# Kernel tuning notes

Hardware: AMD Instinct MI355X
Metric: run time of the kernel (lower is better)

Reference implementation:

```python
import jax, jax.numpy as jnp
import numpy as np

B, N, C, H = 4, 4096, 1024, 16
HD = C // H  # head_dim = 64
EPS = 1e-6


def setup_inputs() -> dict:
    key = jax.random.key(0)
    ks = jax.random.split(key, 5)
    x = jax.random.normal(ks[0], (B, N, C), dtype=jnp.float32)
    s_in = 1.0 / np.sqrt(C)
    W_qkv = jax.random.normal(ks[1], (C, 3 * C), dtype=jnp.float32) * s_in
    b_qkv = jnp.zeros((3 * C,), dtype=jnp.float32)
    W_out = jax.random.normal(ks[2], (C, C), dtype=jnp.float32) * s_in
    b_out = jnp.zeros((C,), dtype=jnp.float32)
    return {"x": x, "W_qkv": W_qkv, "b_qkv": b_qkv, "W_out": W_out, "b_out": b_out}


def reference(x, W_qkv, b_qkv, W_out, b_out):
    # qkv projection: (B, N, 3C)
    qkv = jnp.einsum('bnc,cf->bnf', x, W_qkv) + b_qkv
    # rearrange 'b n (h d) -> b h n d' with d = 3*head_dim, then chunk into q,k,v
    qkv = qkv.reshape(B, N, H, 3 * HD).transpose(0, 2, 1, 3)  # (B,H,N,3*HD)
    q, k, v = jnp.split(qkv, 3, axis=-1)  # each (B,H,N,HD)
    # silu feature map
    q = jax.nn.silu(q)
    k = jax.nn.silu(k)
    # linear attention: state = k^T @ v per head  -> (B,H,HD,HD)
    state = jnp.einsum('bhnd,bhne->bhde', k, v)
    k_sum = k.sum(axis=2)  # (B,H,HD)
    num = jnp.einsum('bhnd,bhde->bhne', q, state)  # (B,H,N,HD)
    den = jnp.einsum('bhnd,bhd->bhn', q, k_sum)[..., None]  # (B,H,N,1)
    out = num / (den + EPS)
    # 'b h n d -> b n (h d)'
    out = out.transpose(0, 2, 1, 3).reshape(B, N, C)
    return jnp.einsum('bnc,cf->bnf', out, W_out) + b_out
```

## Files before the change

kernel.cpp:

```cpp
#include <hip/hip_runtime.h>

typedef unsigned short u16;
typedef unsigned int u32;
typedef __attribute__((ext_vector_type(8))) short short8;
typedef __attribute__((ext_vector_type(8))) _Float16 half8;
typedef __attribute__((ext_vector_type(4))) float f32x4;

#define DEV __device__ __forceinline__

DEV void async_copy16(const void* g, void* l) {
  __builtin_amdgcn_global_load_lds((const __attribute__((address_space(1))) u32*)g,
                                   (__attribute__((address_space(3))) u32*)l, 16, 0, 0);
}
DEV float bf2f(u16 u) { return __uint_as_float(((u32)u) << 16); }
DEV u16 f2bf(float f) {
  u32 x = __float_as_uint(f);
  return (u16)((x + 0x7fffu + ((x >> 16) & 1u)) >> 16);
}
DEV u16 f2h_bits(float f) { _Float16 h = (_Float16)f; return __builtin_bit_cast(u16, h); }
DEV float h2f_bits(u16 b) { return (float)__builtin_bit_cast(_Float16, b); }
DEV float silu_f(float x) { return x / (1.0f + __expf(-x)); }

DEV void stage_tile(const u16* __restrict__ G, size_t grow_base, int k0, u16* L, int t) {
#pragma unroll
  for (int it = 0; it < 2; ++it) {
    int c = t + it * 256;
    int r = c >> 2, j = c & 3;
    int js = j ^ ((r >> 1) & 3);
    async_copy16(G + ((grow_base + (size_t)r) << 10) + k0 + js * 8,
                 (char*)L + (size_t)c * 16);
  }
}
DEV half8 frag(const u16* L, int rr, int lq) {
  int sw = lq ^ ((rr >> 1) & 3);
  return *(const half8*)((const char*)L + (size_t)rr * 64 + sw * 16);
}
DEV short8 frag_s(const u16* L, int rr, int lq) {
  int sw = lq ^ ((rr >> 1) & 3);
  return *(const short8*)((const char*)L + (size_t)rr * 64 + sw * 16);
}
DEV half8 frag64(const u16* L, int rr, int slot) {
  return *(const half8*)(L + (size_t)rr * 64 + ((slot ^ (rr & 7)) * 8));
}

__global__ __launch_bounds__(256) void transpose_k(const float* __restrict__ W,
                                                   u16* __restrict__ Wt,
                                                   int K, int N) {
  __shared__ float s[32][33];
  int t = threadIdx.x;
  int tx = t & 31, ty = t >> 5;
  int ntk = K >> 5;
  int bk = blockIdx.x % ntk, bn = blockIdx.x / ntk;
  int k0 = bk * 32, n0 = bn * 32;
#pragma unroll
  for (int i = 0; i < 4; ++i)
    s[ty + 8 * i][tx] = W[(size_t)(k0 + ty + 8 * i) * N + n0 + tx];
  __syncthreads();
#pragma unroll
  for (int i = 0; i < 4; ++i) {
    int r = ty + 8 * i;
    Wt[(size_t)(n0 + r) * K + k0 + tx] = f2bf(s[tx][r]);
  }
}

__global__ __launch_bounds__(256) void prep(const float* __restrict__ x,
                                            u16* __restrict__ X0, u16* __restrict__ X1,
                                            const float* __restrict__ Wq,
                                            u16* __restrict__ W0t, u16* __restrict__ W1t,
                                            const float* __restrict__ Wo,
                                            u16* __restrict__ WoT) {
  __shared__ float s[32][33];
  int bid = blockIdx.x, t = threadIdx.x;
  if (bid < 16384) {
    int i = (bid * 256 + t) * 4;
    float4 v = *(const float4*)&x[i];
    ushort4 h0, h1;
    h0.x = f2h_bits(v.x); h1.x = f2h_bits((v.x - h2f_bits(h0.x)) * 4096.0f);
    h0.y = f2h_bits(v.y); h1.y = f2h_bits((v.y - h2f_bits(h0.y)) * 4096.0f);
    h0.z = f2h_bits(v.z); h1.z = f2h_bits((v.z - h2f_bits(h0.z)) * 4096.0f);
    h0.w = f2h_bits(v.w); h1.w = f2h_bits((v.w - h2f_bits(h0.w)) * 4096.0f);
    *(ushort4*)&X0[i] = h0;
    *(ushort4*)&X1[i] = h1;
  } else if (bid < 16384 + 3072) {
    int b2 = bid - 16384;
    int tx = t & 31, ty = t >> 5;
    int bk = b2 & 31, bn = b2 >> 5;
    int k0 = bk * 32, n0 = bn * 32;
#pragma unroll
    for (int i = 0; i < 4; ++i)
      s[ty + 8 * i][tx] = Wq[(size_t)(k0 + ty + 8 * i) * 3072 + n0 + tx];
    __syncthreads();
#pragma unroll
    for (int i = 0; i < 4; ++i) {
      int r = ty + 8 * i;
      int col = n0 + r;
      int h = col / 192, rem = col - h * 192;
      int cty = rem >> 6, d = rem & 63;
      int pcol = cty * 1024 + h * 64 + d;
      float v = s[tx][r];
      u16 h0 = f2h_bits(v);
      u16 h1 = f2h_bits((v - h2f_bits(h0)) * 4096.0f);
      size_t o = (size_t)pcol * 1024 + k0 + tx;
      W0t[o] = h0;
      W1t[o] = h1;
    }
  } else {
    int b3 = bid - 19456;
    int tx = t & 31, ty = t >> 5;
    int bk = b3 & 31, bn = b3 >> 5;
    int k0 = bk * 32, n0 = bn * 32;
#pragma unroll
    for (int i = 0; i < 4; ++i)
      s[ty + 8 * i][tx] = Wo[(size_t)(k0 + ty + 8 * i) * 1024 + n0 + tx];
    __syncthreads();
#pragma unroll
    for (int i = 0; i < 4; ++i) {
      int r = ty + 8 * i;
      WoT[(size_t)(n0 + r) * 1024 + k0 + tx] = f2bf(s[tx][r]);
    }
  }
}

__global__ __launch_bounds__(256, 2) void gemm_qk_f16(
    const u16* __restrict__ X0, const u16* __restrict__ X1,
    const u16* __restrict__ W0, const u16* __restrict__ W1,
    const float* __restrict__ bq,
    float* __restrict__ Qf, float* __restrict__ Kf) {
  __shared__ u16 lA0[128 * 32];
  __shared__ u16 lA1[128 * 32];
  __shared__ u16 lB0[128 * 32];
  __shared__ u16 lB1[128 * 32];
  int t = threadIdx.x;
  int w = t >> 6, l = t & 63;
  int wr = w >> 1, wc = w & 1;
  int lr = l & 15, lq = l >> 4;
  int mb = blockIdx.y * 128, nb = blockIdx.x * 128;
  int cty = nb >> 10;
  f32x4 aM[4][4] = {};
  f32x4 aC[4][4] = {};

  for (int k0 = 0; k0 < 1024; k0 += 32) {
#pragma unroll
    for (int it = 0; it < 2; ++it) {
      int c = t + it * 256;
      int r = c >> 2, j = c & 3;
      int js = j ^ ((r >> 1) & 3);
      size_t goA = (((size_t)(mb + r)) << 10) + k0 + js * 8;
      size_t goB = (((size_t)(nb + r)) << 10) + k0 + js * 8;
      async_copy16(X0 + goA, (char*)lA0 + (size_t)c * 16);
      async_copy16(X1 + goA, (char*)lA1 + (size_t)c * 16);
      async_copy16(W0 + goB, (char*)lB0 + (size_t)c * 16);
      async_copy16(W1 + goB, (char*)lB1 + (size_t)c * 16);
    }
    __syncthreads();
    half8 b0[4], b1[4];
#pragma unroll
    for (int nn = 0; nn < 4; ++nn) {
      int rr = wc * 64 + nn * 16 + lr;
      b0[nn] = frag(lB0, rr, lq);
      b1[nn] = frag(lB1, rr, lq);
    }
#pragma unroll
    for (int m = 0; m < 4; ++m) {
      int rr = wr * 64 + m * 16 + lr;
      half8 a0 = frag(lA0, rr, lq);
      half8 a1 = frag(lA1, rr, lq);
#pragma unroll
      for (int nn = 0; nn < 4; ++nn) {
        aM[m][nn] = __builtin_amdgcn_mfma_f32_16x16x32_f16(a0, b0[nn], aM[m][nn], 0, 0, 0);
        aC[m][nn] = __builtin_amdgcn_mfma_f32_16x16x32_f16(a0, b1[nn], aC[m][nn], 0, 0, 0);
        aC[m][nn] = __builtin_amdgcn_mfma_f32_16x16x32_f16(a1, b0[nn], aC[m][nn], 0, 0, 0);
      }
    }
    __syncthreads();
  }

  const float cscale = 2.44140625e-4f;
  float* dst = (cty == 0) ? Qf : Kf;
#pragma unroll
  for (int nn = 0; nn < 4; ++nn) {
    int col = nb + wc * 64 + nn * 16 + lr;
    int h = (col & 1023) >> 6, d0 = col & 63;
    float bias = bq[h * 192 + cty * 64 + d0];
#pragma unroll
    for (int m = 0; m < 4; ++m)
#pragma unroll
      for (int j = 0; j < 4; ++j) {
        int row = mb + wr * 64 + m * 16 + lq * 4 + j;
        int b = row >> 12, n = row & 4095;
        size_t base = (((size_t)(b * 16 + h) * 4096 + n) << 6) + d0;
        float val = aM[m][nn][j] + aC[m][nn][j] * cscale + bias;
        dst[base] = silu_f(val);
      }
  }
}

__global__ __launch_bounds__(256) void gemm_v_f16(
    const u16* __restrict__ X0, const u16* __restrict__ W0,
    const float* __restrict__ bq, u16* __restrict__ Vb) {
  __shared__ u16 lA0[128 * 32];
  __shared__ u16 lB0[128 * 32];
  int t = threadIdx.x;
  int w = t >> 6, l = t & 63;
  int wr = w >> 1, wc = w & 1;
  int lr = l & 15, lq = l >> 4;
  int mb = blockIdx.y * 128, nb = 2048 + blockIdx.x * 128;
  f32x4 aM[4][4] = {};

  for (int k0 = 0; k0 < 1024; k0 += 32) {
    stage_tile(X0, mb, k0, lA0, t);
    stage_tile(W0, nb, k0, lB0, t);
    __syncthreads();
    half8 b0[4];
#pragma unroll
    for (int nn = 0; nn < 4; ++nn) b0[nn] = frag(lB0, wc * 64 + nn * 16 + lr, lq);
#pragma unroll
    for (int m = 0; m < 4; ++m) {
      half8 a0 = frag(lA0, wr * 64 + m * 16 + lr, lq);
#pragma unroll
      for (int nn = 0; nn < 4; ++nn)
        aM[m][nn] = __builtin_amdgcn_mfma_f32_16x16x32_f16(a0, b0[nn], aM[m][nn], 0, 0, 0);
    }
    __syncthreads();
  }
#pragma unroll
  for (int nn = 0; nn < 4; ++nn) {
    int col = nb + wc * 64 + nn * 16 + lr;
    int h = (col & 1023) >> 6, d0 = col & 63;
    float bias = bq[h * 192 + 128 + d0];
#pragma unroll
    for (int m = 0; m < 4; ++m)
#pragma unroll
      for (int j = 0; j < 4; ++j) {
        int row = mb + wr * 64 + m * 16 + lq * 4 + j;
        int b = row >> 12, n = row & 4095;
        size_t base = (((size_t)(b * 16 + h) * 4096 + n) << 6) + d0;
        Vb[base] = f2bf(aM[m][nn][j] + bias);
      }
  }
}

__global__ __launch_bounds__(256) void gemm_qkv(const float* __restrict__ X,
                                                const float* __restrict__ Wq,
                                                const float* __restrict__ bq,
                                                float* __restrict__ Qf,
                                                float* __restrict__ Kf,
                                                u16* __restrict__ Vb) {
  __shared__ float sA[16 * 132];
  __shared__ float sB[16 * 128];
  int t = threadIdx.x;
  int tm = t >> 4, tn = t & 15;
  int mb = blockIdx.y * 128, nb = blockIdx.x * 128;
  float acc[8][8] = {};

  for (int k0 = 0; k0 < 1024; k0 += 16) {
#pragma unroll
    for (int it = 0; it < 2; ++it) {
      int c = t + it * 256;
      int m = c >> 2, kc = (c & 3) * 4;
      float4 v = *(const float4*)&X[(size_t)(mb + m) * 1024 + k0 + kc];
      sA[(kc + 0) * 132 + m] = v.x;
      sA[(kc + 1) * 132 + m] = v.y;
      sA[(kc + 2) * 132 + m] = v.z;
      sA[(kc + 3) * 132 + m] = v.w;
      int kr = c >> 5, nc = (c & 31) * 4;
      async_copy16(&Wq[(size_t)(k0 + kr) * 3072 + nb + nc], (char*)sB + (size_t)c * 16);
    }
    __syncthreads();
#pragma unroll
    for (int k = 0; k < 16; ++k) {
      float4 a0 = *(const float4*)&sA[k * 132 + tm * 8];
      float4 a1 = *(const float4*)&sA[k * 132 + tm * 8 + 4];
      float4 b0 = *(const float4*)&sB[k * 128 + tn * 8];
      float4 b1 = *(const float4*)&sB[k * 128 + tn * 8 + 4];
      const float av[8] = {a0.x, a0.y, a0.z, a0.w, a1.x, a1.y, a1.z, a1.w};
      const float bv[8] = {b0.x, b0.y, b0.z, b0.w, b1.x, b1.y, b1.z, b1.w};
#pragma unroll
      for (int i = 0; i < 8; ++i)
#pragma unroll
        for (int j = 0; j < 8; ++j) acc[i][j] = fmaf(av[i], bv[j], acc[i][j]);
    }
    __syncthreads();
  }

  int c0 = nb + tn * 8;
  int h = c0 / 192, rem = c0 % 192;
  int ty = rem >> 6, d0 = rem & 63;
  float bb[8];
#pragma unroll
  for (int j = 0; j < 8; ++j) bb[j] = bq[c0 + j];
#pragma unroll
  for (int i = 0; i < 8; ++i) {
    int r = mb + tm * 8 + i;
    int b = r >> 12, n = r & 4095;
    size_t base = (((size_t)(b * 16 + h) * 4096 + n) << 6) + d0;
    if (ty == 2) {
      u16 pk[8];
#pragma unroll
      for (int j = 0; j < 8; ++j) pk[j] = f2bf(acc[i][j] + bb[j]);
      *(short8*)&Vb[base] = *(short8*)pk;
    } else {
      float* dst = (ty == 0) ? Qf : Kf;
#pragma unroll
      for (int j = 0; j < 8; ++j) dst[base + j] = silu_f(acc[i][j] + bb[j]);
    }
  }
}

__global__ __launch_bounds__(256) void state_partial(const float* __restrict__ Kf,
                                                     const u16* __restrict__ Vb,
                                                     float* __restrict__ stateP,
                                                     float* __restrict__ ksumP) {
  int bh = blockIdx.y, ch = blockIdx.x, t = threadIdx.x;
  __shared__ float sK[64 * 64];
  __shared__ u16 sV[64 * 64];
  __shared__ float sred[256];
  int n0 = ch * 512;
  size_t base = ((size_t)bh * 4096 + n0) << 6;
  float acc[4][4] = {};
  int te = t & 15, td = t >> 4;
  int kd = t & 63, kq = t >> 6;
  float kacc = 0.0f;

  for (int sc = 0; sc < 8; ++sc) {
    const float* gk = Kf + base + (size_t)sc * 64 * 64;
    const u16* gv = Vb + base + (size_t)sc * 64 * 64;
#pragma unroll
    for (int it = 0; it < 4; ++it)
      async_copy16(gk + (size_t)(t + it * 256) * 4, (char*)sK + (size_t)(t + it * 256) * 16);
#pragma unroll
    for (int it = 0; it < 2; ++it)
      async_copy16(gv + (size_t)(t + it * 256) * 8, (char*)sV + (size_t)(t + it * 256) * 16);
    __syncthreads();
#pragma unroll 4
    for (int n = 0; n < 64; ++n) {
      float4 k4 = *(const float4*)&sK[n * 64 + td * 4];
      const float ka[4] = {k4.x, k4.y, k4.z, k4.w};
      ushort4 vv = *(const ushort4*)&sV[n * 64 + te * 4];
      const float va[4] = {bf2f(vv.x), bf2f(vv.y), bf2f(vv.z), bf2f(vv.w)};
#pragma unroll
      for (int i = 0; i < 4; ++i)
#pragma unroll
        for (int j = 0; j < 4; ++j) acc[i][j] = fmaf(ka[i], va[j], acc[i][j]);
    }
#pragma unroll
    for (int i = 0; i < 16; ++i) kacc += sK[(kq * 16 + i) * 64 + kd];
    __syncthreads();
  }
  size_t pb = ((size_t)bh * 8 + ch) * 4096;
#pragma unroll
  for (int i = 0; i < 4; ++i)
#pragma unroll
    for (int j = 0; j < 4; ++j)
      stateP[pb + (size_t)(td * 4 + i) * 64 + te * 4 + j] = acc[i][j];

  sred[t] = kacc;
  __syncthreads();
  if (t < 64)
    ksumP[((size_t)bh * 8 + ch) * 64 + t] = sred[t] + sred[t + 64] + sred[t + 128] + sred[t + 192];
}

__global__ __launch_bounds__(256) void reduce_state(const float* __restrict__ stateP,
                                                    const float* __restrict__ ksumP,
                                                    u16* __restrict__ sTh,
                                                    float* __restrict__ ksumF) {
  int bh = blockIdx.x, t = threadIdx.x;
#pragma unroll
  for (int i = 0; i < 16; ++i) {
    int idx = t + i * 256;
    float s = 0.0f;
#pragma unroll
    for (int c = 0; c < 8; ++c) s += stateP[((size_t)bh * 8 + c) * 4096 + idx];
    int d = idx >> 6, e = idx & 63;
    sTh[((size_t)bh << 12) + e * 64 + d] = f2h_bits(s);
  }
  if (t < 64) {
    float s = 0.0f;
#pragma unroll
    for (int c = 0; c < 8; ++c) s += ksumP[((size_t)bh * 8 + c) * 64 + t];
    ksumF[(size_t)bh * 64 + t] = s;
  }
}

__global__ __launch_bounds__(256) void attn_mfma(const float* __restrict__ Qf,
                                                 const u16* __restrict__ sTh,
                                                 const float* __restrict__ ksumF,
                                                 u16* __restrict__ outb) {
  __shared__ u16 q16[256 * 64];
  __shared__ u16 sT[64 * 64];
  __shared__ float denp[256 * 4];
  __shared__ float den[256];
  int bh = blockIdx.y, chnk = blockIdx.x, t = threadIdx.x;
  int w = t >> 6, l = t & 63;
  int lr16 = l & 15, lq4 = l >> 4;

  {
    const u16* src = sTh + ((size_t)bh << 12);
#pragma unroll
    for (int it = 0; it < 2; ++it) {
      int c = t + it * 256;
      short8 v = *(const short8*)(src + c * 8);
      int e = c >> 3, slot = c & 7;
      *(short8*)&sT[e * 64 + ((slot ^ (e & 7)) * 8)] = v;
    }
  }
  {
    int quarter = t & 3, rbase = t >> 2;
    float4 skr[4];
#pragma unroll
    for (int i4 = 0; i4 < 4; ++i4)
      skr[i4] = *(const float4*)&ksumF[(size_t)bh * 64 + quarter * 16 + i4 * 4];
#pragma unroll
    for (int p = 0; p < 4; ++p) {
      int row = rbase + p * 64;
      int n = chnk * 256 + row;
      const float* qrow = Qf + (((size_t)bh * 4096 + n) << 6) + quarter * 16;
      float dp = 0.0f;
      u16 h[16];
#pragma unroll
      for (int i4 = 0; i4 < 4; ++i4) {
        float4 v = *(const float4*)(qrow + i4 * 4);
        dp += v.x * skr[i4].x + v.y * skr[i4].y + v.z * skr[i4].z + v.w * skr[i4].w;
        h[i4 * 4 + 0] = f2h_bits(v.x);
        h[i4 * 4 + 1] = f2h_bits(v.y);
        h[i4 * 4 + 2] = f2h_bits(v.z);
        h[i4 * 4 + 3] = f2h_bits(v.w);
      }
      denp[row * 4 + quarter] = dp;
      int s0 = (quarter * 2) ^ (row & 7);
      int s1 = (quarter * 2 + 1) ^ (row & 7);
      *(short8*)&q16[row * 64 + s0 * 8] = *(short8*)&h[0];
      *(short8*)&q16[row * 64 + s1 * 8] = *(short8*)&h[8];
    }
  }
  __syncthreads();
  den[t] = denp[t * 4] + denp[t * 4 + 1] + denp[t * 4 + 2] + denp[t * 4 + 3];
  __syncthreads();

  f32x4 acc[4][4] = {};
#pragma unroll
  for (int kh = 0; kh < 2; ++kh) {
    half8 bfr[4];
#pragma unroll
    for (int nt = 0; nt < 4; ++nt)
      bfr[nt] = frag64(sT, nt * 16 + lr16, kh * 4 + lq4);
#pragma unroll
    for (int rt = 0; rt < 4; ++rt) {
      half8 a = frag64(q16, w * 64 + rt * 16 + lr16, kh * 4 + lq4);
#pragma unroll
      for (int nt = 0; nt < 4; ++nt)
        acc[rt][nt] = __builtin_amdgcn_mfma_f32_16x16x32_f16(a, bfr[nt], acc[rt][nt], 0, 0, 0);
    }
  }

  int b = bh >> 4, hh = bh & 15;
#pragma unroll
  for (int rt = 0; rt < 4; ++rt) {
#pragma unroll
    for (int j = 0; j < 4; ++j) {
      int row = w * 64 + rt * 16 + lq4 * 4 + j;
      float rden = 1.0f / (den[row] + 1e-6f);
      int n = chnk * 256 + row;
      size_t ob = (((size_t)(b * 4096 + n)) << 10) + hh * 64;
#pragma unroll
      for (int nt = 0; nt < 4; ++nt) {
        int e = nt * 16 + lr16;
        outb[ob + e] = f2bf(acc[rt][nt][j] * rden);
      }
    }
  }
}

__global__ __launch_bounds__(256) void gemm_out(const u16* __restrict__ A,
                                                const u16* __restrict__ Bt,
                                                const float* __restrict__ bias,
                                                float* __restrict__ C) {
  __shared__ u16 lA[128 * 32];
  __shared__ u16 lB[128 * 32];
  int t = threadIdx.x;
  int w = t >> 6, l = t & 63;
  int wr = w >> 1, wc = w & 1;
  int lr = l & 15, lq = l >> 4;
  int mb = blockIdx.y * 128, nb = blockIdx.x * 128;
  f32x4 acc[4][4] = {};

  for (int k0 = 0; k0 < 1024; k0 += 32) {
    stage_tile(A, mb, k0, lA, t);
    stage_tile(Bt, nb, k0, lB, t);
    __syncthreads();
    short8 af[4], bf[4];
#pragma unroll
    for (int m = 0; m < 4; ++m) af[m] = frag_s(lA, wr * 64 + m * 16 + lr, lq);
#pragma unroll
    for (int nn = 0; nn < 4; ++nn) bf[nn] = frag_s(lB, wc * 64 + nn * 16 + lr, lq);
#pragma unroll
    for (int m = 0; m < 4; ++m)
#pragma unroll
      for (int nn = 0; nn < 4; ++nn)
        acc[m][nn] = __builtin_amdgcn_mfma_f32_16x16x32_bf16(af[m], bf[nn], acc[m][nn], 0, 0, 0);
    __syncthreads();
  }

#pragma unroll
  for (int m = 0; m < 4; ++m)
#pragma unroll
    for (int nn = 0; nn < 4; ++nn) {
      int col = nb + wc * 64 + nn * 16 + lr;
      float bc = bias[col];
#pragma unroll
      for (int j = 0; j < 4; ++j) {
        int row = mb + wr * 64 + m * 16 + lq * 4 + j;
        C[((size_t)row << 10) + col] = acc[m][nn][j] + bc;
      }
    }
}

extern "C" void kernel_launch(void* const* d_in, const int* in_sizes, int n_in,
                              void* d_out, int out_size, void* d_ws, size_t ws_size,
                              hipStream_t stream) {
  const float* x    = (const float*)d_in[0];
  const float* Wqkv = (const float*)d_in[1];
  const float* bqkv = (const float*)d_in[2];
  const float* Wout = (const float*)d_in[3];
  const float* bout = (const float*)d_in[4];
  float* out = (float*)d_out;

  char* w = (char*)d_ws;
  const size_t offK  = 0;
  const size_t offV  = offK + 67108864ULL;
  const size_t offSP = offV + 33554432ULL;
  const size_t offKP = offSP + 8388608ULL;
  const size_t offWT = offKP + 131072ULL;
  const size_t offST = offWT + 2097152ULL;
  const size_t offKF = offST + 524288ULL;
  const size_t need_base = offKF + 16384ULL;
  const size_t offX0 = need_base;
  const size_t offX1 = offX0 + 33554432ULL;
  const size_t offW0 = offX1 + 33554432ULL;
  const size_t offW1 = offW0 + 6291456ULL;
  const size_t need_fast = offW1 + 6291456ULL;

  if (ws_size < need_base) return;

  float* Kf     = (float*)(w + offK);
  u16*   outb   = (u16*)(w + offK);
  u16*   Vb     = (u16*)(w + offV);
  float* stateP = (float*)(w + offSP);
  float* ksumP  = (float*)(w + offKP);
  u16*   WoutT  = (u16*)(w + offWT);
  u16*   sTh    = (u16*)(w + offST);
  float* ksumF  = (float*)(w + offKF);
  float* Qf     = out;

  if (ws_size >= need_fast) {
    u16* X0 = (u16*)(w + offX0);
    u16* X1 = (u16*)(w + offX1);
    u16* W0 = (u16*)(w + offW0);
    u16* W1 = (u16*)(w + offW1);
    prep<<<dim3(20480), dim3(256), 0, stream>>>(x, X0, X1, Wqkv, W0, W1, Wout, WoutT);
    gemm_qk_f16<<<dim3(16, 128), dim3(256), 0, stream>>>(X0, X1, W0, W1, bqkv, Qf, Kf);
    gemm_v_f16<<<dim3(8, 128), dim3(256), 0, stream>>>(X0, W0, bqkv, Vb);
  } else {
    transpose_k<<<dim3(1024), dim3(256), 0, stream>>>(Wout, WoutT, 1024, 1024);
    gemm_qkv<<<dim3(24, 128), dim3(256), 0, stream>>>(x, Wqkv, bqkv, Qf, Kf, Vb);
  }

  state_partial<<<dim3(8, 64), dim3(256), 0, stream>>>(Kf, Vb, stateP, ksumP);
  reduce_state<<<dim3(64), dim3(256), 0, stream>>>(stateP, ksumP, sTh, ksumF);
  attn_mfma<<<dim3(16, 64), dim3(256), 0, stream>>>(Qf, sTh, ksumF, outb);
  gemm_out<<<dim3(8, 128), dim3(256), 0, stream>>>(outb, WoutT, bout, out);
}
```

Measured before the change: 433.0 us.

## Store K and V transposed in bf16 and compute state with MFMA

The QK GEMM epilogue now writes K as transposed bf16 (head-dim major) instead of fp32, and computes per-tile column sums of K into a partial ksum buffer. The V GEMM writes V transposed too. A new state_mfma kernel computes K^T V with bf16 MFMA from these layouts, replacing the scalar state_partial kernel on the fast path. This cuts K traffic in half and moves the state product onto matrix cores, at the cost of bf16 rounding on K and a different workspace layout.

```diff
diff --git a/kernel.cpp b/kernel.cpp
--- a/kernel.cpp
+++ b/kernel.cpp
@@ -125,7 +125,7 @@
     const u16* __restrict__ X0, const u16* __restrict__ X1,
     const u16* __restrict__ W0, const u16* __restrict__ W1,
     const float* __restrict__ bq,
-    float* __restrict__ Qf, float* __restrict__ Kf) {
+    float* __restrict__ Qf, u16* __restrict__ Kt, float* __restrict__ ksumP2) {
   __shared__ u16 lA0[128 * 32];
   __shared__ u16 lA1[128 * 32];
   __shared__ u16 lB0[128 * 32];
@@ -176,28 +176,63 @@
   }
 
   const float cscale = 2.44140625e-4f;
-  float* dst = (cty == 0) ? Qf : Kf;
-#pragma unroll
-  for (int nn = 0; nn < 4; ++nn) {
-    int col = nb + wc * 64 + nn * 16 + lr;
-    int h = (col & 1023) >> 6, d0 = col & 63;
-    float bias = bq[h * 192 + cty * 64 + d0];
-#pragma unroll
-    for (int m = 0; m < 4; ++m)
-#pragma unroll
-      for (int j = 0; j < 4; ++j) {
-        int row = mb + wr * 64 + m * 16 + lq * 4 + j;
-        int b = row >> 12, n = row & 4095;
-        size_t base = (((size_t)(b * 16 + h) * 4096 + n) << 6) + d0;
-        float val = aM[m][nn][j] + aC[m][nn][j] * cscale + bias;
-        dst[base] = silu_f(val);
+  if (cty == 0) {
+#pragma unroll
+    for (int nn = 0; nn < 4; ++nn) {
+      int col = nb + wc * 64 + nn * 16 + lr;
+      int h = (col & 1023) >> 6, d0 = col & 63;
+      float bias = bq[h * 192 + d0];
+#pragma unroll
+      for (int m = 0; m < 4; ++m)
+#pragma unroll
+        for (int j = 0; j < 4; ++j) {
+          int row = mb + wr * 64 + m * 16 + lq * 4 + j;
+          int b = row >> 12, n = row & 4095;
+          size_t base = (((size_t)(b * 16 + h) * 4096 + n) << 6) + d0;
+          float val = aM[m][nn][j] + aC[m][nn][j] * cscale + bias;
+          Qf[base] = silu_f(val);
+        }
+    }
+  } else {
+    float* red = (float*)lA0;
+    int b = mb >> 12, nbase = mb & 4095;
+#pragma unroll
+    for (int nn = 0; nn < 4; ++nn) {
+      int clocal = wc * 64 + nn * 16 + lr;
+      int colk = (nb - 1024) + clocal;
+      int h = colk >> 6, d0 = colk & 63;
+      float bias = bq[h * 192 + 64 + d0];
+      size_t krow = (((size_t)(b * 16 + h) * 64 + d0) << 12) + nbase + wr * 64;
+      float lsum = 0.0f;
+#pragma unroll
+      for (int m = 0; m < 4; ++m) {
+        ushort4 pk;
+        float v0 = silu_f(aM[m][nn][0] + aC[m][nn][0] * cscale + bias);
+        float v1 = silu_f(aM[m][nn][1] + aC[m][nn][1] * cscale + bias);
+        float v2 = silu_f(aM[m][nn][2] + aC[m][nn][2] * cscale + bias);
+        float v3 = silu_f(aM[m][nn][3] + aC[m][nn][3] * cscale + bias);
+        lsum += v0 + v1 + v2 + v3;
+        pk.x = f2bf(v0); pk.y = f2bf(v1); pk.z = f2bf(v2); pk.w = f2bf(v3);
+        *(ushort4*)&Kt[krow + m * 16 + lq * 4] = pk;
       }
+      red[clocal * 8 + wr * 4 + lq] = lsum;
+    }
+    __syncthreads();
+    if (t < 128) {
+      float s = 0.0f;
+#pragma unroll
+      for (int c = 0; c < 8; ++c) s += red[t * 8 + c];
+      int colk = (nb - 1024) + t;
+      int h = colk >> 6, d0 = colk & 63;
+      int rowtile = blockIdx.y & 31;
+      ksumP2[(((size_t)(b * 16 + h) * 64 + d0) << 5) + rowtile] = s;
+    }
   }
 }
 
 __global__ __launch_bounds__(256) void gemm_v_f16(
     const u16* __restrict__ X0, const u16* __restrict__ W0,
-    const float* __restrict__ bq, u16* __restrict__ Vb) {
+    const float* __restrict__ bq, u16* __restrict__ Vt) {
   __shared__ u16 lA0[128 * 32];
   __shared__ u16 lB0[128 * 32];
   int t = threadIdx.x;
@@ -223,21 +258,226 @@
     }
     __syncthreads();
   }
+  int b = mb >> 12, nbase = mb & 4095;
 #pragma unroll
   for (int nn = 0; nn < 4; ++nn) {
-    int col = nb + wc * 64 + nn * 16 + lr;
-    int h = (col & 1023) >> 6, d0 = col & 63;
-    float bias = bq[h * 192 + 128 + d0];
+    int colv = (nb - 2048) + wc * 64 + nn * 16 + lr;
+    int h = colv >> 6, e0 = colv & 63;
+    float bias = bq[h * 192 + 128 + e0];
+    size_t vrow = (((size_t)(b * 16 + h) * 64 + e0) << 12) + nbase + wr * 64;
+#pragma unroll
+    for (int m = 0; m < 4; ++m) {
+      ushort4 pk;
+      pk.x = f2bf(aM[m][nn][0] + bias);
+      pk.y = f2bf(aM[m][nn][1] + bias);
+      pk.z = f2bf(aM[m][nn][2] + bias);
+      pk.w = f2bf(aM[m][nn][3] + bias);
+      *(ushort4*)&Vt[vrow + m * 16 + lq * 4] = pk;
+    }
+  }
+}
+
+__global__ __launch_bounds__(256) void state_mfma(const u16* __restrict__ Kt,
+                                                  const u16* __restrict__ Vt,
+                                                  float* __restrict__ stateP) {
+  __shared__ u16 sA[64 * 32];
+  __shared__ u16 sB[64 * 32];
+  int bh = blockIdx.y, ch = blockIdx.x, t = threadIdx.x;
+  int w = t >> 6, l = t & 63;
+  int wr = w >> 1, wc = w & 1;
+  int lr = l & 15, lq = l >> 4;
+  size_t rb = (size_t)bh << 6;
+  f32x4 acc[2][2] = {};
+
+  for (int n0 = ch * 512; n0 < ch * 512 + 512; n0 += 32) {
+    {
+      int c = t;
+      int r = c >> 2, j = c & 3;
+      int js = j ^ ((r >> 1) & 3);
+      size_t go = ((rb + (size_t)r) << 12) + n0 + js * 8;
+      async_copy16(Kt + go, (char*)sA + (size_t)c * 16);
+      async_copy16(Vt + go, (char*)sB + (size_t)c * 16);
+    }
+    __syncthreads();
+    short8 bfr[2];
+#pragma unroll
+    for (int nn = 0; nn < 2; ++nn) bfr[nn] = frag_s(sB, wc * 32 + nn * 16 + lr, lq);
+#pragma unroll
+    for (int m = 0; m < 2; ++m) {
+      short8 a = frag_s(sA, wr * 32 + m * 16 + lr, lq);
+#pragma unroll
+      for (int nn = 0; nn < 2; ++nn)
+        acc[m][nn] = __builtin_amdgcn_mfma_f32_16x16x32_bf16(a, bfr[nn], acc[m][nn], 0, 0, 0);
+    }
+    __syncthreads();
+  }
+
+  size_t pb = ((size_t)bh * 8 + ch) * 4096;
+#pragma unroll
+  for (int m = 0; m < 2; ++m)
+#pragma unroll
+    for (int nn = 0; nn < 2; ++nn)
+#pragma unroll
+      for (int j = 0; j < 4; ++j) {
+        int d = wr * 32 + m * 16 + lq * 4 + j;
+        int e = wc * 32 + nn * 16 + lr;
+        stateP[pb + (size_t)d * 64 + e] = acc[m][nn][j];
+      }
+}
+
+__global__ __launch_bounds__(256) void reduce_state2(const float* __restrict__ stateP,
+                                                     const float* __restrict__ ksumP2,
+                                                     u16* __restrict__ sTh,
+                                                     float* __restrict__ ksumF) {
+  int bh = blockIdx.x, t = threadIdx.x;
+#pragma unroll
+  for (int i = 0; i < 16; ++i) {
+    int idx = t + i * 256;
+    float s = 0.0f;
+#pragma unroll
+    for (int c = 0; c < 8; ++c) s += stateP[((size_t)bh * 8 + c) * 4096 + idx];
+    int d = idx >> 6, e = idx & 63;
+    sTh[((size_t)bh << 12) + e * 64 + d] = f2h_bits(s);
+  }
+  if (t < 64) {
+    float s = 0.0f;
+#pragma unroll
+    for (int c = 0; c < 32; ++c) s += ksumP2[(((size_t)bh * 64 + t) << 5) + c];
+    ksumF[(size_t)bh * 64 + t] = s;
+  }
+}
+
+__global__ __launch_bounds__(256) void attn_mfma(const float* __restrict__ Qf,
+                                                 const u16* __restrict__ sTh,
+                                                 const float* __restrict__ ksumF,
+                                                 u16* __restrict__ outb) {
+  __shared__ u16 q16[256 * 64];
+  __shared__ u16 sT[64 * 64];
+  __shared__ float denp[256 * 4];
+  __shared__ float den[256];
+  int bh = blockIdx.y, chnk = blockIdx.x, t = threadIdx.x;
+  int w = t >> 6, l = t & 63;
+  int lr16 = l & 15, lq4 = l >> 4;
+
+  {
+    const u16* src = sTh + ((size_t)bh << 12);
+#pragma unroll
+    for (int it = 0; it < 2; ++it) {
+      int c = t + it * 256;
+      short8 v = *(const short8*)(src + c * 8);
+      int e = c >> 3, slot = c & 7;
+      *(short8*)&sT[e * 64 + ((slot ^ (e & 7)) * 8)] = v;
+    }
+  }
+  {
+    int quarter = t & 3, rbase = t >> 2;
+    float4 skr[4];
+#pragma unroll
+    for (int i4 = 0; i4 < 4; ++i4)
+      skr[i4] = *(const float4*)&ksumF[(size_t)bh * 64 + quarter * 16 + i4 * 4];
+#pragma unroll
+    for (int p = 0; p < 4; ++p) {
+      int row = rbase + p * 64;
+      int n = chnk * 256 + row;
+      const float* qrow = Qf + (((size_t)bh * 4096 + n) << 6) + quarter * 16;
+      float dp = 0.0f;
+      u16 h[16];
+#pragma unroll
+      for (int i4 = 0; i4 < 4; ++i4) {
+        float4 v = *(const float4*)(qrow + i4 * 4);
+        dp += v.x * skr[i4].x + v.y * skr[i4].y + v.z * skr[i4].z + v.w * skr[i4].w;
+        h[i4 * 4 + 0] = f2h_bits(v.x);
+        h[i4 * 4 + 1] = f2h_bits(v.y);
+        h[i4 * 4 + 2] = f2h_bits(v.z);
+        h[i4 * 4 + 3] = f2h_bits(v.w);
+      }
+      denp[row * 4 + quarter] = dp;
+      int s0 = (quarter * 2) ^ (row & 7);
+      int s1 = (quarter * 2 + 1) ^ (row & 7);
+      *(short8*)&q16[row * 64 + s0 * 8] = *(short8*)&h[0];
+      *(short8*)&q16[row * 64 + s1 * 8] = *(short8*)&h[8];
+    }
+  }
+  __syncthreads();
+  den[t] = denp[t * 4] + denp[t * 4 + 1] + denp[t * 4 + 2] + denp[t * 4 + 3];
+  __syncthreads();
+
+  f32x4 acc[4][4] = {};
+#pragma unroll
+  for (int kh = 0; kh < 2; ++kh) {
+    half8 bfr[4];
+#pragma unroll
+    for (int nt = 0; nt < 4; ++nt)
+      bfr[nt] = frag64(sT, nt * 16 + lr16, kh * 4 + lq4);
+#pragma unroll
+    for (int rt = 0; rt < 4; ++rt) {
+      half8 a = frag64(q16, w * 64 + rt * 16 + lr16, kh * 4 + lq4);
+#pragma unroll
+      for (int nt = 0; nt < 4; ++nt)
+        acc[rt][nt] = __builtin_amdgcn_mfma_f32_16x16x32_f16(a, bfr[nt], acc[rt][nt], 0, 0, 0);
+    }
+  }
+
+  int b = bh >> 4, hh = bh & 15;
+#pragma unroll
+  for (int rt = 0; rt < 4; ++rt) {
+#pragma unroll
+    for (int j = 0; j < 4; ++j) {
+      int row = w * 64 + rt * 16 + lq4 * 4 + j;
+      float rden = 1.0f / (den[row] + 1e-6f);
+      int n = chnk * 256 + row;
+      size_t ob = (((size_t)(b * 4096 + n)) << 10) + hh * 64;
+#pragma unroll
+      for (int nt = 0; nt < 4; ++nt) {
+        int e = nt * 16 + lr16;
+        outb[ob + e] = f2bf(acc[rt][nt][j] * rden);
+      }
+    }
+  }
+}
+
+__global__ __launch_bounds__(256) void gemm_out(const u16* __restrict__ A,
+                                                const u16* __restrict__ Bt,
+                                                const float* __restrict__ bias,
+                                                float* __restrict__ C) {
+  __shared__ u16 lA[128 * 32];
+  __shared__ u16 lB[128 * 32];
+  int t = threadIdx.x;
+  int w = t >> 6, l = t & 63;
+  int wr = w >> 1, wc = w & 1;
+  int lr = l & 15, lq = l >> 4;
+  int mb = blockIdx.y * 128, nb = blockIdx.x * 128;
+  f32x4 acc[4][4] = {};
+
+  for (int k0 = 0; k0 < 1024; k0 += 32) {
+    stage_tile(A, mb, k0, lA, t);
+    stage_tile(Bt, nb, k0, lB, t);
+    __syncthreads();
+    short8 af[4], bf[4];
+#pragma unroll
+    for (int m = 0; m < 4; ++m) af[m] = frag_s(lA, wr * 64 + m * 16 + lr, lq);
+#pragma unroll
+    for (int nn = 0; nn < 4; ++nn) bf[nn] = frag_s(lB, wc * 64 + nn * 16 + lr, lq);
 #pragma unroll
     for (int m = 0; m < 4; ++m)
+#pragma unroll
+      for (int nn = 0; nn < 4; ++nn)
+        acc[m][nn] = __builtin_amdgcn_mfma_f32_16x16x32_bf16(af[m], bf[nn], acc[m][nn], 0, 0, 0);
+    __syncthreads();
+  }
+
+#pragma unroll
+  for (int m = 0; m < 4; ++m)
+#pragma unroll
+    for (int nn = 0; nn < 4; ++nn) {
+      int col = nb + wc * 64 + nn * 16 + lr;
+      float bc = bias[col];
 #pragma unroll
       for (int j = 0; j < 4; ++j) {
         int row = mb + wr * 64 + m * 16 + lq * 4 + j;
-        int b = row >> 12, n = row & 4095;
-        size_t base = (((size_t)(b * 16 + h) * 4096 + n) << 6) + d0;
-        Vb[base] = f2bf(aM[m][nn][j] + bias);
+        C[((size_t)row << 10) + col] = acc[m][nn][j] + bc;
       }
-  }
+    }
 }
 
 __global__ __launch_bounds__(256) void gemm_qkv(const float* __restrict__ X,
@@ -360,10 +600,10 @@
     ksumP[((size_t)bh * 8 + ch) * 64 + t] = sred[t] + sred[t + 64] + sred[t + 128] + sred[t + 192];
 }
 
-__global__ __launch_bounds__(256) void reduce_state(const float* __restrict__ stateP,
-                                                    const float* __restrict__ ksumP,
-                                                    u16* __restrict__ sTh,
-                                                    float* __restrict__ ksumF) {
+__global__ __launch_bounds__(256) void reduce_state_fb(const float* __restrict__ stateP,
+                                                       const float* __restrict__ ksumP,
+                                                       u16* __restrict__ sTh,
+                                                       float* __restrict__ ksumF) {
   int bh = blockIdx.x, t = threadIdx.x;
 #pragma unroll
   for (int i = 0; i < 16; ++i) {
@@ -380,139 +620,6 @@
     for (int c = 0; c < 8; ++c) s += ksumP[((size_t)bh * 8 + c) * 64 + t];
     ksumF[(size_t)bh * 64 + t] = s;
   }
-}
-
-__global__ __launch_bounds__(256) void attn_mfma(const float* __restrict__ Qf,
-                                                 const u16* __restrict__ sTh,
-                                                 const float* __restrict__ ksumF,
-                                                 u16* __restrict__ outb) {
-  __shared__ u16 q16[256 * 64];
-  __shared__ u16 sT[64 * 64];
-  __shared__ float denp[256 * 4];
-  __shared__ float den[256];
-  int bh = blockIdx.y, chnk = blockIdx.x, t = threadIdx.x;
-  int w = t >> 6, l = t & 63;
-  int lr16 = l & 15, lq4 = l >> 4;
-
-  {
-    const u16* src = sTh + ((size_t)bh << 12);
-#pragma unroll
-    for (int it = 0; it < 2; ++it) {
-      int c = t + it * 256;
-      short8 v = *(const short8*)(src + c * 8);
-      int e = c >> 3, slot = c & 7;
-      *(short8*)&sT[e * 64 + ((slot ^ (e & 7)) * 8)] = v;
-    }
-  }
-  {
-    int quarter = t & 3, rbase = t >> 2;
-    float4 skr[4];
-#pragma unroll
-    for (int i4 = 0; i4 < 4; ++i4)
-      skr[i4] = *(const float4*)&ksumF[(size_t)bh * 64 + quarter * 16 + i4 * 4];
-#pragma unroll
-    for (int p = 0; p < 4; ++p) {
-      int row = rbase + p * 64;
-      int n = chnk * 256 + row;
-      const float* qrow = Qf + (((size_t)bh * 4096 + n) << 6) + quarter * 16;
-      float dp = 0.0f;
-      u16 h[16];
-#pragma unroll
-      for (int i4 = 0; i4 < 4; ++i4) {
-        float4 v = *(const float4*)(qrow + i4 * 4);
-        dp += v.x * skr[i4].x + v.y * skr[i4].y + v.z * skr[i4].z + v.w * skr[i4].w;
-        h[i4 * 4 + 0] = f2h_bits(v.x);
-        h[i4 * 4 + 1] = f2h_bits(v.y);
-        h[i4 * 4 + 2] = f2h_bits(v.z);
-        h[i4 * 4 + 3] = f2h_bits(v.w);
-      }
-      denp[row * 4 + quarter] = dp;
-      int s0 = (quarter * 2) ^ (row & 7);
-      int s1 = (quarter * 2 + 1) ^ (row & 7);
-      *(short8*)&q16[row * 64 + s0 * 8] = *(short8*)&h[0];
-      *(short8*)&q16[row * 64 + s1 * 8] = *(short8*)&h[8];
-    }
-  }
-  __syncthreads();
-  den[t] = denp[t * 4] + denp[t * 4 + 1] + denp[t * 4 + 2] + denp[t * 4 + 3];
-  __syncthreads();
-
-  f32x4 acc[4][4] = {};
-#pragma unroll
-  for (int kh = 0; kh < 2; ++kh) {
-    half8 bfr[4];
-#pragma unroll
-    for (int nt = 0; nt < 4; ++nt)
-      bfr[nt] = frag64(sT, nt * 16 + lr16, kh * 4 + lq4);
-#pragma unroll
-    for (int rt = 0; rt < 4; ++rt) {
-      half8 a = frag64(q16, w * 64 + rt * 16 + lr16, kh * 4 + lq4);
-#pragma unroll
-      for (int nt = 0; nt < 4; ++nt)
-        acc[rt][nt] = __builtin_amdgcn_mfma_f32_16x16x32_f16(a, bfr[nt], acc[rt][nt], 0, 0, 0);
-    }
-  }
-
-  int b = bh >> 4, hh = bh & 15;
-#pragma unroll
-  for (int rt = 0; rt < 4; ++rt) {
-#pragma unroll
-    for (int j = 0; j < 4; ++j) {
-      int row = w * 64 + rt * 16 + lq4 * 4 + j;
-      float rden = 1.0f / (den[row] + 1e-6f);
-      int n = chnk * 256 + row;
-      size_t ob = (((size_t)(b * 4096 + n)) << 10) + hh * 64;
-#pragma unroll
-      for (int nt = 0; nt < 4; ++nt) {
-        int e = nt * 16 + lr16;
-        outb[ob + e] = f2bf(acc[rt][nt][j] * rden);
-      }
-    }
-  }
-}
-
-__global__ __launch_bounds__(256) void gemm_out(const u16* __restrict__ A,
-                                                const u16* __restrict__ Bt,
-                                                const float* __restrict__ bias,
-                                                float* __restrict__ C) {
-  __shared__ u16 lA[128 * 32];
-  __shared__ u16 lB[128 * 32];
-  int t = threadIdx.x;
-  int w = t >> 6, l = t & 63;
-  int wr = w >> 1, wc = w & 1;
-  int lr = l & 15, lq = l >> 4;
-  int mb = blockIdx.y * 128, nb = blockIdx.x * 128;
-  f32x4 acc[4][4] = {};
-
-  for (int k0 = 0; k0 < 1024; k0 += 32) {
-    stage_tile(A, mb, k0, lA, t);
-    stage_tile(Bt, nb, k0, lB, t);
-    __syncthreads();
-    short8 af[4], bf[4];
-#pragma unroll
-    for (int m = 0; m < 4; ++m) af[m] = frag_s(lA, wr * 64 + m * 16 + lr, lq);
-#pragma unroll
-    for (int nn = 0; nn < 4; ++nn) bf[nn] = frag_s(lB, wc * 64 + nn * 16 + lr, lq);
-#pragma unroll
-    for (int m = 0; m < 4; ++m)
-#pragma unroll
-      for (int nn = 0; nn < 4; ++nn)
-        acc[m][nn] = __builtin_amdgcn_mfma_f32_16x16x32_bf16(af[m], bf[nn], acc[m][nn], 0, 0, 0);
-    __syncthreads();
-  }
-
-#pragma unroll
-  for (int m = 0; m < 4; ++m)
-#pragma unroll
-    for (int nn = 0; nn < 4; ++nn) {
-      int col = nb + wc * 64 + nn * 16 + lr;
-      float bc = bias[col];
-#pragma unroll
-      for (int j = 0; j < 4; ++j) {
-        int row = mb + wr * 64 + m * 16 + lq * 4 + j;
-        C[((size_t)row << 10) + col] = acc[m][nn][j] + bc;
-      }
-    }
 }
 
 extern "C" void kernel_launch(void* const* d_in, const int* in_sizes, int n_in,
@@ -526,47 +633,67 @@
   float* out = (float*)d_out;
 
   char* w = (char*)d_ws;
-  const size_t offK  = 0;
-  const size_t offV  = offK + 67108864ULL;
-  const size_t offSP = offV + 33554432ULL;
-  const size_t offKP = offSP + 8388608ULL;
-  const size_t offWT = offKP + 131072ULL;
-  const size_t offST = offWT + 2097152ULL;
-  const size_t offKF = offST + 524288ULL;
-  const size_t need_base = offKF + 16384ULL;
-  const size_t offX0 = need_base;
-  const size_t offX1 = offX0 + 33554432ULL;
-  const size_t offW0 = offX1 + 33554432ULL;
-  const size_t offW1 = offW0 + 6291456ULL;
-  const size_t need_fast = offW1 + 6291456ULL;
-
-  if (ws_size < need_base) return;
-
-  float* Kf     = (float*)(w + offK);
-  u16*   outb   = (u16*)(w + offK);
-  u16*   Vb     = (u16*)(w + offV);
-  float* stateP = (float*)(w + offSP);
-  float* ksumP  = (float*)(w + offKP);
-  u16*   WoutT  = (u16*)(w + offWT);
-  u16*   sTh    = (u16*)(w + offST);
-  float* ksumF  = (float*)(w + offKF);
-  float* Qf     = out;
+
+  const size_t fKT  = 0;
+  const size_t fVT  = fKT  + 33554432ULL;
+  const size_t fSP  = fVT  + 33554432ULL;
+  const size_t fKP2 = fSP  + 8388608ULL;
+  const size_t fWT  = fKP2 + 524288ULL;
+  const size_t fST  = fWT  + 2097152ULL;
+  const size_t fKF  = fST  + 524288ULL;
+  const size_t fX0  = fKF  + 16384ULL;
+  const size_t fX1  = fX0  + 33554432ULL;
+  const size_t fW0  = fX1  + 33554432ULL;
+  const size_t fW1  = fW0  + 6291456ULL;
+  const size_t need_fast = fW1 + 6291456ULL;
+
+  const size_t bK  = 0;
+  const size_t bV  = bK + 67108864ULL;
+  const size_t bSP = bV + 33554432ULL;
+  const size_t bKP = bSP + 8388608ULL;
+  const size_t bWT = bKP + 131072ULL;
+  const size_t bST = bWT + 2097152ULL;
+  const size_t bKF = bST + 524288ULL;
+  const size_t need_base = bKF + 16384ULL;
 
   if (ws_size >= need_fast) {
-    u16* X0 = (u16*)(w + offX0);
-    u16* X1 = (u16*)(w + offX1);
-    u16* W0 = (u16*)(w + offW0);
-    u16* W1 = (u16*)(w + offW1);
+    u16*   Kt     = (u16*)(w + fKT);
+    u16*   outb   = (u16*)(w + fKT);
+    u16*   Vt     = (u16*)(w + fVT);
+    float* stateP = (float*)(w + fSP);
+    float* ksumP2 = (float*)(w + fKP2);
+    u16*   WoutT  = (u16*)(w + fWT);
+    u16*   sTh    = (u16*)(w + fST);
+    float* ksumF  = (float*)(w + fKF);
+    u16*   X0     = (u16*)(w + fX0);
+    u16*   X1     = (u16*)(w + fX1);
+    u16*   W0     = (u16*)(w + fW0);
+    u16*   W1     = (u16*)(w + fW1);
+    float* Qf     = out;
+
     prep<<<dim3(20480), dim3(256), 0, stream>>>(x, X0, X1, Wqkv, W0, W1, Wout, WoutT);
-    gemm_qk_f16<<<dim3(16, 128), dim3(256), 0, stream>>>(X0, X1, W0, W1, bqkv, Qf, Kf);
-    gemm_v_f16<<<dim3(8, 128), dim3(256), 0, stream>>>(X0, W0, bqkv, Vb);
-  } else {
+    gemm_qk_f16<<<dim3(16, 128), dim3(256), 0, stream>>>(X0, X1, W0, W1, bqkv, Qf, Kt, ksumP2);
+    gemm_v_f16<<<dim3(8, 128), dim3(256), 0, stream>>>(X0, W0, bqkv, Vt);
+    state_mfma<<<dim3(8, 64), dim3(256), 0, stream>>>(Kt, Vt, stateP);
+    reduce_state2<<<dim3(64), dim3(256), 0, stream>>>(stateP, ksumP2, sTh, ksumF);
+    attn_mfma<<<dim3(16, 64), dim3(256), 0, stream>>>(Qf, sTh, ksumF, outb);
+    gemm_out<<<dim3(8, 128), dim3(256), 0, stream>>>(outb, WoutT, bout, out);
+  } else if (ws_size >= need_base) {
+    float* Kf     = (float*)(w + bK);
+    u16*   outb   = (u16*)(w + bK);
+    u16*   Vb     = (u16*)(w + bV);
+    float* stateP = (float*)(w + bSP);
+    float* ksumP  = (float*)(w + bKP);
+    u16*   WoutT  = (u16*)(w + bWT);
+    u16*   sTh    = (u16*)(w + bST);
+    float* ksumF  = (float*)(w + bKF);
+    float* Qf     = out;
+
     transpose_k<<<dim3(1024), dim3(256), 0, stream>>>(Wout, WoutT, 1024, 1024);
     gemm_qkv<<<dim3(24, 128), dim3(256), 0, stream>>>(x, Wqkv, bqkv, Qf, Kf, Vb);
-  }
-
-  state_partial<<<dim3(8, 64), dim3(256), 0, stream>>>(Kf, Vb, stateP, ksumP);
-  reduce_state<<<dim3(64), dim3(256), 0, stream>>>(stateP, ksumP, sTh, ksumF);
-  attn_mfma<<<dim3(16, 64), dim3(256), 0, stream>>>(Qf, sTh, ksumF, outb);
-  gemm_out<<<dim3(8, 128), dim3(256), 0, stream>>>(outb, WoutT, bout, out);
-}
+    state_partial<<<dim3(8, 64), dim3(256), 0, stream>>>(Kf, Vb, stateP, ksumP);
+    reduce_state_fb<<<dim3(64), dim3(256), 0, stream>>>(stateP, ksumP, sTh, ksumF);
+    attn_mfma<<<dim3(16, 64), dim3(256), 0, stream>>>(Qf, sTh, ksumF, outb);
+    gemm_out<<<dim3(8, 128), dim3(256), 0, stream>>>(outb, WoutT, bout, out);
+  }
+}
```

After: 396.4 us. -8.5%, faster.
